# Kernel tuning notes

Hardware: AMD Instinct MI355X
Metric: run time of the kernel (lower is better)

The kernel has to match this reference:

```python
import jax, jax.numpy as jnp
import numpy as np

N_NODES = 50000
N_EDGES = 800000
NODE_IN = 16
NODE_OUT = 3
H = 128
N_LAYERS = 3


def setup_inputs() -> dict:
    key = jax.random.key(0)
    ks = jax.random.split(key, 16)
    s = 0.05
    inp = {
        "x": jax.random.normal(ks[0], (N_NODES, NODE_IN), dtype=jnp.float32),
        "edge_index": jax.random.randint(ks[1], (2, N_EDGES), 0, N_NODES, dtype=jnp.int64),
        # encoder / decoder
        "enc_w": jax.random.normal(ks[2], (NODE_IN, H), dtype=jnp.float32) * s,
        "enc_b": jnp.zeros((H,), dtype=jnp.float32),
        "dec_w": jax.random.normal(ks[3], (H, NODE_OUT), dtype=jnp.float32) * s,
        "dec_b": jnp.zeros((NODE_OUT,), dtype=jnp.float32),
        # 3 processor layers, edge MLP: Linear(2H,H) -> ReLU -> Linear(H,H)
        "edge_w1": jax.random.normal(ks[4], (N_LAYERS, 2 * H, H), dtype=jnp.float32) * s,
        "edge_b1": jnp.zeros((N_LAYERS, H), dtype=jnp.float32),
        "edge_w2": jax.random.normal(ks[5], (N_LAYERS, H, H), dtype=jnp.float32) * s,
        "edge_b2": jnp.zeros((N_LAYERS, H), dtype=jnp.float32),
        # node MLP: Linear(2H,H) -> ReLU -> Linear(H,H)
        "node_w1": jax.random.normal(ks[6], (N_LAYERS, 2 * H, H), dtype=jnp.float32) * s,
        "node_b1": jnp.zeros((N_LAYERS, H), dtype=jnp.float32),
        "node_w2": jax.random.normal(ks[7], (N_LAYERS, H, H), dtype=jnp.float32) * s,
        "node_b2": jnp.zeros((N_LAYERS, H), dtype=jnp.float32),
    }
    return inp


def reference(x, edge_index, enc_w, enc_b, dec_w, dec_b,
              edge_w1, edge_b1, edge_w2, edge_b2,
              node_w1, node_b1, node_w2, node_b2):
    row = edge_index[0]  # source nodes
    col = edge_index[1]  # destination nodes
    h = x @ enc_w + enc_b  # [N, H]
    for l in range(N_LAYERS):
        # EdgeModel: cat(src, dest) -> MLP
        e_in = jnp.concatenate([h[row], h[col]], axis=1)  # [E, 2H]
        e = jnp.maximum(e_in @ edge_w1[l] + edge_b1[l], 0.0) @ edge_w2[l] + edge_b2[l]  # [E, H]
        # NodeModel: scatter_add messages by col, cat with x -> MLP
        agg = jax.ops.segment_sum(e, col, num_segments=h.shape[0])  # [N, H]
        n_in = jnp.concatenate([h, agg], axis=1)  # [N, 2H]
        h_upd = jnp.maximum(n_in @ node_w1[l] + node_b1[l], 0.0) @ node_w2[l] + node_b2[l]
        h = h + h_upd  # residual
    return h @ dec_w + dec_b  # [N, NODE_OUT]
```

## Files before the change

kernel.cpp:

```cpp
#include <hip/hip_runtime.h>
#include <hip/hip_bf16.h>
#include <stdint.h>

#define N_NODES 50000
#define N_EDGES 800000
#define HID 128
#define NODE_IN 16
#define NODE_OUT 3
#define NODE_TILES 782
#define SCAN_BLOCKS 196
#define EDGE_BLOCKS 3125
#define MFOLD_BLOCKS 192
#define SWZA_BLOCKS 576
#define SWZB_BLOCKS 384
#define EDBLOCKS 6250

typedef __attribute__((ext_vector_type(8))) short short8;
typedef __attribute__((ext_vector_type(4))) float f32x4;
typedef __attribute__((ext_vector_type(4))) unsigned int u32x4;

__device__ __forceinline__ unsigned short f2bf(float f) {
    union { float f; unsigned int u; } v; v.f = f;
    unsigned int u = v.u;
    u += 0x7fff + ((u >> 16) & 1);
    return (unsigned short)(u >> 16);
}
__device__ __forceinline__ float bf2f(unsigned short s) {
    union { unsigned int u; float f; } v; v.u = ((unsigned int)s) << 16;
    return v.f;
}
__device__ __forceinline__ float bfu_lo(unsigned int u) {
    union { unsigned int u; float f; } v; v.u = u << 16; return v.f;
}
__device__ __forceinline__ float bfu_hi(unsigned int u) {
    union { unsigned int u; float f; } v; v.u = u & 0xffff0000u; return v.f;
}
__device__ __forceinline__ unsigned int cvt_pk_bf16(float lo, float hi) {
    unsigned int r;
    asm("v_cvt_pk_bf16_f32 %0, %1, %2" : "=v"(r) : "v"(lo), "v"(hi));
    return r;
}

__global__ __launch_bounds__(256) void k1_fused(
    const int* __restrict__ colp, int* __restrict__ cnt8, int* __restrict__ rank,
    const float* __restrict__ edge_w2, const float* __restrict__ node_w1,
    const float* __restrict__ edge_b2,
    float* __restrict__ Mtmp, float* __restrict__ Vtmp,
    const float* __restrict__ x, const float* __restrict__ enc_w,
    const float* __restrict__ enc_b, unsigned short* __restrict__ h,
    const float* __restrict__ edge_w1, const float* __restrict__ node_w2,
    unsigned short* __restrict__ swz,
    const float* __restrict__ eb1,
    unsigned short* __restrict__ S, unsigned short* __restrict__ D) {
    __shared__ float wts[NODE_IN * HID];
    __shared__ float bts[HID];
    __shared__ float xs[64][NODE_IN];
    __shared__ unsigned short hs[64][136];
    int b = blockIdx.x, t = threadIdx.x;
    if (b < EDGE_BLOCKS) {
        int e = b * 256 + t;
        int c = colp[e];
        rank[e] = atomicAdd(&cnt8[(size_t)(b & 7) * N_NODES + c], 1);
    } else if (b < EDGE_BLOCKS + MFOLD_BLOCKS) {
        int d = (b - EDGE_BLOCKS) * 256 + t;
        int L = d / 16384, rem = d & 16383;
        int k = rem >> 7, n = rem & 127;
        const float* w2  = edge_w2 + (size_t)L * 16384;
        const float* w1b = node_w1 + (size_t)L * 32768 + 16384;
        float acc = 0.f;
        #pragma unroll 4
        for (int j = 0; j < 128; j++) acc += w2[k * 128 + j] * w1b[j * 128 + n];
        Mtmp[d] = acc;
        if (k == 0) {
            const float* b2 = edge_b2 + (size_t)L * 128;
            float vv = 0.f;
            #pragma unroll 4
            for (int j = 0; j < 128; j++) vv += b2[j] * w1b[j * 128 + n];
            Vtmp[L * 128 + n] = vv;
        }
    } else if (b < EDGE_BLOCKS + MFOLD_BLOCKS + NODE_TILES) {
        int b2 = b - EDGE_BLOCKS - MFOLD_BLOCKS;
        int wave = t >> 6, l = t & 63, q = l >> 4, l16 = l & 15;
        int nt0s = wave * 4;
        int n0 = b2 * 64;

        for (int i = t; i < NODE_IN * HID; i += 256) wts[i] = enc_w[i];
        if (t < HID) bts[t] = enc_b[t];
        for (int i = t; i < 64 * NODE_IN; i += 256) {
            int nl = i >> 4, ii = i & 15;
            int n = n0 + nl;
            xs[nl][ii] = (n < N_NODES) ? x[n * NODE_IN + ii] : 0.f;
        }
        short8 wr[4][4];
        #pragma unroll
        for (int kt = 0; kt < 4; kt++)
            #pragma unroll
            for (int i = 0; i < 4; i++) {
                int ccol = (nt0s + i) * 16 + l16;
                #pragma unroll
                for (int j = 0; j < 8; j++) {
                    int k = kt * 32 + ((l >> 4) << 3) + j;
                    float v = (ccol < 128) ? edge_w1[k * 128 + ccol]
                                           : edge_w1[(128 + k) * 128 + (ccol - 128)];
                    ((unsigned short*)&wr[kt][i])[j] = f2bf(v);
                }
            }
        __syncthreads();

        for (int o = t; o < 64 * HID; o += 256) {
            int nl = o >> 7, cc = o & 127;
            float acc = bts[cc];
            #pragma unroll
            for (int i = 0; i < NODE_IN; i++) acc += xs[nl][i] * wts[i * HID + cc];
            unsigned short hb = f2bf(acc);
            hs[nl][cc] = hb;
            int n = n0 + nl;
            if (n < N_NODES) h[n * HID + cc] = hb;
        }
        __syncthreads();

        f32x4 acc[4][4];
        #pragma unroll
        for (int g = 0; g < 4; g++)
            #pragma unroll
            for (int i = 0; i < 4; i++) acc[g][i] = (f32x4){0.f, 0.f, 0.f, 0.f};
        #pragma unroll
        for (int kt = 0; kt < 4; kt++) {
            #pragma unroll
            for (int g = 0; g < 4; g++) {
                short8 a = *(const short8*)&hs[g * 16 + l16][kt * 32 + q * 8];
                #pragma unroll
                for (int i = 0; i < 4; i++)
                    acc[g][i] = __builtin_amdgcn_mfma_f32_16x16x32_bf16(a, wr[kt][i], acc[g][i], 0, 0, 0);
            }
        }
        #pragma unroll
        for (int i = 0; i < 4; i++) {
            int cc = (nt0s + i) * 16 + l16;
            float badd = 0.f;
            if (cc >= 128) badd = eb1[cc - 128];
            #pragma unroll
            for (int g = 0; g < 4; g++)
                #pragma unroll
                for (int r = 0; r < 4; r++) {
                    int n = n0 + g * 16 + q * 4 + r;
                    if (n < N_NODES) {
                        unsigned short v = f2bf(acc[g][i][r] + badd);
                        if (cc < 128) S[n * HID + cc] = v;
                        else          D[n * HID + (cc - 128)] = v;
                    }
                }
        }
    } else {
        int d = (b - EDGE_BLOCKS - MFOLD_BLOCKS - NODE_TILES) * 256 + t;
        int L = d / 49152, rem2 = d - L * 49152;
        unsigned short* base = swz + L * 98304;
        if (rem2 < 32768) {
            const float* w1 = edge_w1 + (size_t)L * 32768;
            int j = rem2 & 7, ll = (rem2 >> 3) & 63, tt = rem2 >> 9;
            int nt = tt & 15, kt = tt >> 4;
            int k = kt * 32 + ((ll >> 4) << 3) + j;
            int cc = nt * 16 + (ll & 15);
            float v = (cc < 128) ? w1[k * 128 + cc] : w1[(128 + k) * 128 + (cc - 128)];
            base[rem2] = f2bf(v);
        } else {
            int d2 = rem2 - 32768;
            const float* src = node_w2 + (size_t)L * 16384;
            int j = d2 & 7, ll = (d2 >> 3) & 63, tt = d2 >> 9;
            int nt = tt & 7, kt = tt >> 3;
            int k = kt * 32 + ((ll >> 4) << 3) + j, n = (nt << 4) + (ll & 15);
            base[81920 + d2] = f2bf(src[k * 128 + n]);
        }
    }
}

__global__ __launch_bounds__(256) void k2a_scan1_swizzle(
    const int* __restrict__ cnt8, int* __restrict__ base8, int* __restrict__ cntt,
    int* __restrict__ ex, int* __restrict__ bsums,
    const float* __restrict__ node_w1, const float* __restrict__ Mtmp,
    unsigned short* __restrict__ swz) {
    __shared__ int s[256];
    int b = blockIdx.x, t = threadIdx.x;
    if (b < SCAN_BLOCKS) {
        int i = b * 256 + t;
        int tot = 0;
        if (i < N_NODES) {
            #pragma unroll
            for (int s2 = 0; s2 < 8; s2++) {
                int v = cnt8[(size_t)s2 * N_NODES + i];
                base8[(size_t)s2 * N_NODES + i] = tot;
                tot += v;
            }
            cntt[i] = tot;
        }
        s[t] = tot;
        __syncthreads();
        for (int off = 1; off < 256; off <<= 1) {
            int u = (t >= off) ? s[t - off] : 0;
            __syncthreads();
            s[t] += u;
            __syncthreads();
        }
        if (i < N_NODES) ex[i] = s[t] - tot;
        if (t == 255) bsums[b] = s[255];
    } else {
        int d = (b - SCAN_BLOCKS) * 256 + t;
        int L = d / 32768, d2 = d - L * 32768;
        unsigned short* base = swz + L * 98304;
        int j = d2 & 7, ll = (d2 >> 3) & 63, tt = d2 >> 9;
        int nt = tt & 7, kt = tt >> 3;
        int k = kt * 32 + ((ll >> 4) << 3) + j, n = (nt << 4) + (ll & 15);
        float v = (k < 128) ? node_w1[(size_t)L * 32768 + k * 128 + n]
                            : Mtmp[(size_t)L * 16384 + (k - 128) * 128 + n];
        base[49152 + d2] = f2bf(v);
    }
}

__global__ __launch_bounds__(256) void k3_scatter(
    const int* __restrict__ rowp, const int* __restrict__ colp,
    const int* __restrict__ ex, const int* __restrict__ bsums,
    const int* __restrict__ rank, const int* __restrict__ base8,
    int* __restrict__ rsrt, int* __restrict__ ex2) {
    __shared__ int sc[256];
    __shared__ int ls[SCAN_BLOCKS];
    int b = blockIdx.x, t = threadIdx.x;
    int v = (t < SCAN_BLOCKS) ? bsums[t] : 0;
    sc[t] = v;
    __syncthreads();
    for (int off = 1; off < 256; off <<= 1) {
        int u = (t >= off) ? sc[t - off] : 0;
        __syncthreads();
        sc[t] += u;
        __syncthreads();
    }
    if (t < SCAN_BLOCKS) ls[t] = sc[t] - v;
    __syncthreads();

    if (b < SCAN_BLOCKS) {
        int i = b * 256 + t;
        if (i < N_NODES) ex2[i] = ex[i] + ls[b];
    }
    int e = b * 256 + t;
    int c = colp[e];
    int sh = b & 7;
    int pos = ex[c] + ls[c >> 8] + base8[(size_t)sh * N_NODES + c] + rank[e];
    rsrt[pos] = rowp[e];
}

__global__ __launch_bounds__(256, 8) void edge_kernel(
    const unsigned short* __restrict__ S, const unsigned short* __restrict__ D,
    const int* __restrict__ rsrt, const int* __restrict__ ex2,
    unsigned short* __restrict__ aggB)
{
    int t = threadIdx.x;
    int g32 = t >> 5, ch = t & 31;

    const int q = EDBLOCKS / 8, r = EDBLOCKS % 8;
    int xcd = blockIdx.x & 7, slot = blockIdx.x >> 3;
    int cntx = q + (xcd < r);
    if (slot >= cntx) return;
    int myb = xcd * q + (xcd < r ? xcd : r) + slot;

    int d = myb * 8 + g32;
    int e0 = ex2[d];
    int e1 = (d < N_NODES - 1) ? ex2[d + 1] : N_EDGES;

    int2 dv = *(const int2*)(D + (size_t)d * HID + ch * 4);
    float dr0 = bfu_lo((unsigned int)dv.x), dr1 = bfu_hi((unsigned int)dv.x);
    float dr2 = bfu_lo((unsigned int)dv.y), dr3 = bfu_hi((unsigned int)dv.y);
    float a0 = 0.f, a1 = 0.f, a2 = 0.f, a3 = 0.f;

    auto Srow = [&](int rn) -> int2 {
        return *(const int2*)(S + (size_t)rn * HID + ch * 4);
    };
    auto accum = [&](int2 sv) {
        float v0 = bfu_lo((unsigned int)sv.x) + dr0;
        float v1 = bfu_hi((unsigned int)sv.x) + dr1;
        float v2 = bfu_lo((unsigned int)sv.y) + dr2;
        float v3 = bfu_hi((unsigned int)sv.y) + dr3;
        a0 += v0 > 0.f ? v0 : 0.f;
        a1 += v1 > 0.f ? v1 : 0.f;
        a2 += v2 > 0.f ? v2 : 0.f;
        a3 += v3 > 0.f ? v3 : 0.f;
    };
    const int2 z = make_int2(0, 0);

    int2 c0 = z, c1 = z, c2 = z, c3 = z;
    int rb0 = 0, rb1 = 0, rb2 = 0, rb3 = 0;
    {
        int ra0 = (e0     < e1) ? rsrt[e0]     : 0;
        int ra1 = (e0 + 1 < e1) ? rsrt[e0 + 1] : 0;
        int ra2 = (e0 + 2 < e1) ? rsrt[e0 + 2] : 0;
        int ra3 = (e0 + 3 < e1) ? rsrt[e0 + 3] : 0;
        rb0 = (e0 + 4 < e1) ? rsrt[e0 + 4] : 0;
        rb1 = (e0 + 5 < e1) ? rsrt[e0 + 5] : 0;
        rb2 = (e0 + 6 < e1) ? rsrt[e0 + 6] : 0;
        rb3 = (e0 + 7 < e1) ? rsrt[e0 + 7] : 0;
        if (e0     < e1) c0 = Srow(ra0);
        if (e0 + 1 < e1) c1 = Srow(ra1);
        if (e0 + 2 < e1) c2 = Srow(ra2);
        if (e0 + 3 < e1) c3 = Srow(ra3);
    }

    int e = e0;
    while (e + 12 <= e1) {
        int m0 = rsrt[e + 8], m1 = rsrt[e + 9];
        int2 f0 = Srow(rb0), f1 = Srow(rb1);
        accum(c0); accum(c1);
        int m2 = rsrt[e + 10], m3 = rsrt[e + 11];
        int2 f2 = Srow(rb2), f3 = Srow(rb3);
        accum(c2); accum(c3);
        c0 = f0; c1 = f1; c2 = f2; c3 = f3;
        rb0 = m0; rb1 = m1; rb2 = m2; rb3 = m3;
        e += 4;
    }
    int rem = e1 - e;
    if (rem > 0) accum(c0);
    if (rem > 1) accum(c1);
    if (rem > 2) accum(c2);
    if (rem > 3) accum(c3);
    if (rem > 4) accum(Srow(rb0));
    if (rem > 5) accum(Srow(rb1));
    if (rem > 6) accum(Srow(rb2));
    if (rem > 7) accum(Srow(rb3));
    for (int j = 8; j < rem; j++) accum(Srow(rsrt[e + j]));

    int2 o = make_int2((int)cvt_pk_bf16(a0, a1), (int)cvt_pk_bf16(a2, a3));
    *(int2*)(aggB + (size_t)d * HID + ch * 4) = o;
}

template<int LAST>
__global__ __launch_bounds__(256, 4) void node_kernel(
    unsigned short* __restrict__ h, const unsigned short* __restrict__ aggB,
    const int* __restrict__ cnt,
    const unsigned short* __restrict__ w1m_s, const float* __restrict__ b1,
    const float* __restrict__ vfold,
    const unsigned short* __restrict__ w2s, const float* __restrict__ b2,
    const unsigned short* __restrict__ w1c_next, const float* __restrict__ eb1n,
    unsigned short* __restrict__ S, unsigned short* __restrict__ D,
    const float* __restrict__ dec_w, const float* __restrict__ dec_b, float* __restrict__ out)
{
    __shared__ unsigned short in_h[64][136];
    __shared__ unsigned short in_a[64][136];
    __shared__ int cnt_s[64];
    __shared__ float dw[HID * NODE_OUT];
    __shared__ float db[NODE_OUT];
    int t = threadIdx.x, wave = t >> 6, l = t & 63, q = l >> 4, l16 = l & 15;
    int nt0 = wave * 2, nt0s = wave * 4;
    int n0 = blockIdx.x * 64;

    if (LAST) {
        for (int i = t; i < HID * NODE_OUT; i += 256) dw[i] = dec_w[i];
        if (t < NODE_OUT) db[t] = dec_b[t];
    }

    #pragma unroll
    for (int it = 0; it < 8; it++) {
        int g = it * 256 + t;
        int nl = g >> 5, sub = g & 31, half = sub >> 4, li = sub & 15;
        int n = n0 + nl;
        short8 v = (short8){0, 0, 0, 0, 0, 0, 0, 0};
        if (n < N_NODES) {
            if (half == 0) v = *(const short8*)(h + (size_t)n * HID + li * 8);
            else           v = *(const short8*)(aggB + (size_t)n * HID + li * 8);
        }
        if (half == 0) *(short8*)&in_h[nl][li * 8] = v;
        else           *(short8*)&in_a[nl][li * 8] = v;
    }
    if (t < 64) cnt_s[t] = (n0 + t < N_NODES) ? cnt[n0 + t] : 0;
    __syncthreads();

    float b1r0 = b1[nt0 * 16 + l16], b1r1 = b1[(nt0 + 1) * 16 + l16];
    float vr0 = vfold[nt0 * 16 + l16], vr1 = vfold[(nt0 + 1) * 16 + l16];
    float b2r0 = b2[nt0 * 16 + l16], b2r1 = b2[(nt0 + 1) * 16 + l16];

    f32x4 acc[4][2];
    #pragma unroll
    for (int g = 0; g < 4; g++)
        #pragma unroll
        for (int j = 0; j < 2; j++) acc[g][j] = (f32x4){0.f, 0.f, 0.f, 0.f};
    #pragma unroll
    for (int kt = 0; kt < 8; kt++) {
        short8 b0 = *(const short8*)(w1m_s + ((kt * 8 + nt0)     * 64 + l) * 8);
        short8 b1v = *(const short8*)(w1m_s + ((kt * 8 + nt0 + 1) * 64 + l) * 8);
        #pragma unroll
        for (int g = 0; g < 4; g++) {
            short8 a = (kt < 4) ? *(const short8*)&in_h[g * 16 + l16][kt * 32 + q * 8]
                                : *(const short8*)&in_a[g * 16 + l16][(kt - 4) * 32 + q * 8];
            acc[g][0] = __builtin_amdgcn_mfma_f32_16x16x32_bf16(a, b0, acc[g][0], 0, 0, 0);
            acc[g][1] = __builtin_amdgcn_mfma_f32_16x16x32_bf16(a, b1v, acc[g][1], 0, 0, 0);
        }
    }
    __syncthreads();

    #pragma unroll
    for (int j = 0; j < 2; j++) {
        float bv = j ? b1r1 : b1r0;
        float vv = j ? vr1 : vr0;
        #pragma unroll
        for (int g = 0; g < 4; g++)
            #pragma unroll
            for (int r = 0; r < 4; r++) {
                int m2 = g * 16 + q * 4 + r;
                float v = acc[g][j][r] + bv + (float)cnt_s[m2] * vv;
                v = v > 0.f ? v : 0.f;
                in_a[m2][(nt0 + j) * 16 + l16] = f2bf(v);
            }
    }
    __syncthreads();

    f32x4 acc2[4][2];
    #pragma unroll
    for (int g = 0; g < 4; g++)
        #pragma unroll
        for (int j = 0; j < 2; j++) acc2[g][j] = (f32x4){0.f, 0.f, 0.f, 0.f};
    #pragma unroll
    for (int kt = 0; kt < 4; kt++) {
        short8 b0 = *(const short8*)(w2s + ((kt * 8 + nt0)     * 64 + l) * 8);
        short8 b1v = *(const short8*)(w2s + ((kt * 8 + nt0 + 1) * 64 + l) * 8);
        #pragma unroll
        for (int g = 0; g < 4; g++) {
            short8 a = *(const short8*)&in_a[g * 16 + l16][kt * 32 + q * 8];
            acc2[g][0] = __builtin_amdgcn_mfma_f32_16x16x32_bf16(a, b0, acc2[g][0], 0, 0, 0);
            acc2[g][1] = __builtin_amdgcn_mfma_f32_16x16x32_bf16(a, b1v, acc2[g][1], 0, 0, 0);
        }
    }
    #pragma unroll
    for (int j = 0; j < 2; j++) {
        float bv = j ? b2r1 : b2r0;
        #pragma unroll
        for (int g = 0; g < 4; g++)
            #pragma unroll
            for (int r = 0; r < 4; r++) {
                float v = acc2[g][j][r] + bv;
                int m2 = g * 16 + q * 4 + r;
                int n = n0 + m2;
                if (n < N_NODES) {
                    int c = (nt0 + j) * 16 + l16;
                    unsigned short nh = f2bf(bf2f(in_h[m2][c]) + v);
                    if (!LAST) h[n * HID + c] = nh;
                    in_h[m2][c] = nh;
                }
            }
    }
    __syncthreads();

    if (!LAST) {
        #pragma unroll
        for (int p = 0; p < 2; p++) {
            short8 wr[4][2];
            #pragma unroll
            for (int kt = 0; kt < 4; kt++) {
                wr[kt][0] = *(const short8*)(w1c_next + ((kt * 16 + nt0s + p * 2)     * 64 + l) * 8);
                wr[kt][1] = *(const short8*)(w1c_next + ((kt * 16 + nt0s + p * 2 + 1) * 64 + l) * 8);
            }
            f32x4 accs[4][2];
            #pragma unroll
            for (int g = 0; g < 4; g++)
                #pragma unroll
                for (int i = 0; i < 2; i++) accs[g][i] = (f32x4){0.f, 0.f, 0.f, 0.f};
            #pragma unroll
            for (int kt = 0; kt < 4; kt++) {
                #pragma unroll
                for (int g = 0; g < 4; g++) {
                    short8 a = *(const short8*)&in_h[g * 16 + l16][kt * 32 + q * 8];
                    accs[g][0] = __builtin_amdgcn_mfma_f32_16x16x32_bf16(a, wr[kt][0], accs[g][0], 0, 0, 0);
                    accs[g][1] = __builtin_amdgcn_mfma_f32_16x16x32_bf16(a, wr[kt][1], accs[g][1], 0, 0, 0);
                }
            }
            #pragma unroll
            for (int i = 0; i < 2; i++) {
                int c = (nt0s + p * 2 + i) * 16 + l16;
                float badd = 0.f;
                if (c >= 128) badd = eb1n[c - 128];
                #pragma unroll
                for (int g = 0; g < 4; g++)
                    #pragma unroll
                    for (int r = 0; r < 4; r++) {
                        int n = n0 + g * 16 + q * 4 + r;
                        if (n < N_NODES) {
                            unsigned short v = f2bf(accs[g][i][r] + badd);
                            if (c < 128) S[n * HID + c] = v;
                            else         D[n * HID + (c - 128)] = v;
                        }
                    }
            }
        }
    } else {
        if (t < 64 * NODE_OUT) {
            int nl = t / 3, o = t - 3 * nl;
            int n = n0 + nl;
            if (n < N_NODES) {
                float a = db[o];
                #pragma unroll 4
                for (int k = 0; k < HID; k++) a += bf2f(in_h[nl][k]) * dw[k * 3 + o];
                out[n * 3 + o] = a;
            }
        }
    }
}

extern "C" void kernel_launch(void* const* d_in, const int* in_sizes, int n_in,
                              void* d_out, int out_size, void* d_ws, size_t ws_size,
                              hipStream_t stream) {
    const float* x       = (const float*)d_in[0];
    const int*   ei      = (const int*)d_in[1];
    const float* enc_w   = (const float*)d_in[2];
    const float* enc_b   = (const float*)d_in[3];
    const float* dec_w   = (const float*)d_in[4];
    const float* dec_b   = (const float*)d_in[5];
    const float* edge_w1 = (const float*)d_in[6];
    const float* edge_b1 = (const float*)d_in[7];
    const float* edge_w2 = (const float*)d_in[8];
    const float* edge_b2 = (const float*)d_in[9];
    const float* node_w1 = (const float*)d_in[10];
    const float* node_b1 = (const float*)d_in[11];
    const float* node_w2 = (const float*)d_in[12];
    const float* node_b2 = (const float*)d_in[13];

    char* ws = (char*)d_ws;
    unsigned short* h    = (unsigned short*)ws;
    unsigned short* aggB = (unsigned short*)(ws + 12800000);
    unsigned short* swz  = (unsigned short*)(ws + 25600000);
    int* cnt8            = (int*)(ws + 26189824);
    int* base8           = (int*)(ws + 27789824);
    int* cntt            = (int*)(ws + 29389824);
    int* ex              = (int*)(ws + 29589824);
    int* bsums           = (int*)(ws + 29789824);
    int* rsrt            = (int*)(ws + 29790848);
    unsigned short* Sbuf = (unsigned short*)(ws + 32990848);
    unsigned short* Dbuf = (unsigned short*)(ws + 45790848);
    float* Mtmp          = (float*)(ws + 58590848);
    float* Vtmp          = (float*)(ws + 58787456);
    int* ex2             = (int*)(ws + 58788992);
    int* rank            = (int*)(ws + 58988992);

    const int* rowp = ei;
    const int* colp = ei + N_EDGES;

    hipMemsetAsync(cnt8, 0, (size_t)8 * N_NODES * 4, stream);

    k1_fused<<<EDGE_BLOCKS + MFOLD_BLOCKS + NODE_TILES + SWZA_BLOCKS, 256, 0, stream>>>(
        colp, cnt8, rank, edge_w2, node_w1, edge_b2, Mtmp, Vtmp,
        x, enc_w, enc_b, h, edge_w1, node_w2, swz,
        edge_b1 , Sbuf, Dbuf);
    k2a_scan1_swizzle<<<SCAN_BLOCKS + SWZB_BLOCKS, 256, 0, stream>>>(
        cnt8, base8, cntt, ex, bsums, node_w1, Mtmp, swz);
    k3_scatter<<<EDGE_BLOCKS, 256, 0, stream>>>(
        rowp, colp, ex, bsums, rank, base8, rsrt, ex2);

    for (int L = 0; L < 3; L++) {
        unsigned short* base = swz + (size_t)L * 98304;
        unsigned short* next = swz + (size_t)(L + 1) * 98304;
        edge_kernel<<<6256, 256, 0, stream>>>(Sbuf, Dbuf, rsrt, ex2, aggB);
        if (L < 2) {
            node_kernel<0><<<NODE_TILES, 256, 0, stream>>>(
                h, aggB, cntt,
                base + 49152, node_b1 + (size_t)L * HID, Vtmp + (size_t)L * HID,
                base + 81920, node_b2 + (size_t)L * HID,
                next, edge_b1 + (size_t)(L + 1) * HID, Sbuf, Dbuf, dec_w, dec_b, (float*)d_out);
        } else {
            node_kernel<1><<<NODE_TILES, 256, 0, stream>>>(
                h, aggB, cntt,
                base + 49152, node_b1 + (size_t)L * HID, Vtmp + (size_t)L * HID,
                base + 81920, node_b2 + (size_t)L * HID,
                base , edge_b1 , Sbuf, Dbuf, dec_w, dec_b, (float*)d_out);
        }
    }
}
```

Baseline: 361.5 us.

## Move first-layer S/D projection from k1 into scatter kernel using pre-swizzled weights

The layer-0 node-side edge projection (h times edge_w1 halves, producing S and D) moves out of the encoder blocks of k1_fused and into extra blocks appended to the scatter kernel. The new blocks reload the bf16 h from global memory and read weight fragments directly from the pre-swizzled swz buffer built in k1, instead of gathering and converting fp32 edge_w1 per thread. This lightens k1's node-tile blocks, which had expensive strided weight loads and a large MFMA section, and balances work into k3. The cost is an extra global round-trip for h and a heavier k3 launch.

```diff
diff --git a/kernel.cpp b/kernel.cpp
--- a/kernel.cpp
+++ b/kernel.cpp
@@ -49,13 +49,10 @@
     const float* __restrict__ x, const float* __restrict__ enc_w,
     const float* __restrict__ enc_b, unsigned short* __restrict__ h,
     const float* __restrict__ edge_w1, const float* __restrict__ node_w2,
-    unsigned short* __restrict__ swz,
-    const float* __restrict__ eb1,
-    unsigned short* __restrict__ S, unsigned short* __restrict__ D) {
+    unsigned short* __restrict__ swz) {
     __shared__ float wts[NODE_IN * HID];
     __shared__ float bts[HID];
     __shared__ float xs[64][NODE_IN];
-    __shared__ unsigned short hs[64][136];
     int b = blockIdx.x, t = threadIdx.x;
     if (b < EDGE_BLOCKS) {
         int e = b * 256 + t;
@@ -80,10 +77,7 @@
         }
     } else if (b < EDGE_BLOCKS + MFOLD_BLOCKS + NODE_TILES) {
         int b2 = b - EDGE_BLOCKS - MFOLD_BLOCKS;
-        int wave = t >> 6, l = t & 63, q = l >> 4, l16 = l & 15;
-        int nt0s = wave * 4;
         int n0 = b2 * 64;
-
         for (int i = t; i < NODE_IN * HID; i += 256) wts[i] = enc_w[i];
         if (t < HID) bts[t] = enc_b[t];
         for (int i = t; i < 64 * NODE_IN; i += 256) {
@@ -91,65 +85,14 @@
             int n = n0 + nl;
             xs[nl][ii] = (n < N_NODES) ? x[n * NODE_IN + ii] : 0.f;
         }
-        short8 wr[4][4];
-        #pragma unroll
-        for (int kt = 0; kt < 4; kt++)
-            #pragma unroll
-            for (int i = 0; i < 4; i++) {
-                int ccol = (nt0s + i) * 16 + l16;
-                #pragma unroll
-                for (int j = 0; j < 8; j++) {
-                    int k = kt * 32 + ((l >> 4) << 3) + j;
-                    float v = (ccol < 128) ? edge_w1[k * 128 + ccol]
-                                           : edge_w1[(128 + k) * 128 + (ccol - 128)];
-                    ((unsigned short*)&wr[kt][i])[j] = f2bf(v);
-                }
-            }
         __syncthreads();
-
         for (int o = t; o < 64 * HID; o += 256) {
             int nl = o >> 7, cc = o & 127;
             float acc = bts[cc];
             #pragma unroll
             for (int i = 0; i < NODE_IN; i++) acc += xs[nl][i] * wts[i * HID + cc];
-            unsigned short hb = f2bf(acc);
-            hs[nl][cc] = hb;
             int n = n0 + nl;
-            if (n < N_NODES) h[n * HID + cc] = hb;
-        }
-        __syncthreads();
-
-        f32x4 acc[4][4];
-        #pragma unroll
-        for (int g = 0; g < 4; g++)
-            #pragma unroll
-            for (int i = 0; i < 4; i++) acc[g][i] = (f32x4){0.f, 0.f, 0.f, 0.f};
-        #pragma unroll
-        for (int kt = 0; kt < 4; kt++) {
-            #pragma unroll
-            for (int g = 0; g < 4; g++) {
-                short8 a = *(const short8*)&hs[g * 16 + l16][kt * 32 + q * 8];
-                #pragma unroll
-                for (int i = 0; i < 4; i++)
-                    acc[g][i] = __builtin_amdgcn_mfma_f32_16x16x32_bf16(a, wr[kt][i], acc[g][i], 0, 0, 0);
-            }
-        }
-        #pragma unroll
-        for (int i = 0; i < 4; i++) {
-            int cc = (nt0s + i) * 16 + l16;
-            float badd = 0.f;
-            if (cc >= 128) badd = eb1[cc - 128];
-            #pragma unroll
-            for (int g = 0; g < 4; g++)
-                #pragma unroll
-                for (int r = 0; r < 4; r++) {
-                    int n = n0 + g * 16 + q * 4 + r;
-                    if (n < N_NODES) {
-                        unsigned short v = f2bf(acc[g][i][r] + badd);
-                        if (cc < 128) S[n * HID + cc] = v;
-                        else          D[n * HID + (cc - 128)] = v;
-                    }
-                }
+            if (n < N_NODES) h[n * HID + cc] = f2bf(acc);
         }
     } else {
         int d = (b - EDGE_BLOCKS - MFOLD_BLOCKS - NODE_TILES) * 256 + t;
@@ -216,35 +159,93 @@
     }
 }
 
-__global__ __launch_bounds__(256) void k3_scatter(
+__global__ __launch_bounds__(256) void k3_scatter_sd(
     const int* __restrict__ rowp, const int* __restrict__ colp,
     const int* __restrict__ ex, const int* __restrict__ bsums,
     const int* __restrict__ rank, const int* __restrict__ base8,
-    int* __restrict__ rsrt, int* __restrict__ ex2) {
+    int* __restrict__ rsrt, int* __restrict__ ex2,
+    const unsigned short* __restrict__ h, const unsigned short* __restrict__ w1c,
+    const float* __restrict__ eb1,
+    unsigned short* __restrict__ S, unsigned short* __restrict__ D) {
     __shared__ int sc[256];
     __shared__ int ls[SCAN_BLOCKS];
+    __shared__ unsigned short hs[64][136];
     int b = blockIdx.x, t = threadIdx.x;
-    int v = (t < SCAN_BLOCKS) ? bsums[t] : 0;
-    sc[t] = v;
-    __syncthreads();
-    for (int off = 1; off < 256; off <<= 1) {
-        int u = (t >= off) ? sc[t - off] : 0;
+    if (b < EDGE_BLOCKS) {
+        int v = (t < SCAN_BLOCKS) ? bsums[t] : 0;
+        sc[t] = v;
         __syncthreads();
-        sc[t] += u;
+        for (int off = 1; off < 256; off <<= 1) {
+            int u = (t >= off) ? sc[t - off] : 0;
+            __syncthreads();
+            sc[t] += u;
+            __syncthreads();
+        }
+        if (t < SCAN_BLOCKS) ls[t] = sc[t] - v;
         __syncthreads();
-    }
-    if (t < SCAN_BLOCKS) ls[t] = sc[t] - v;
-    __syncthreads();
-
-    if (b < SCAN_BLOCKS) {
-        int i = b * 256 + t;
-        if (i < N_NODES) ex2[i] = ex[i] + ls[b];
-    }
-    int e = b * 256 + t;
-    int c = colp[e];
-    int sh = b & 7;
-    int pos = ex[c] + ls[c >> 8] + base8[(size_t)sh * N_NODES + c] + rank[e];
-    rsrt[pos] = rowp[e];
+
+        if (b < SCAN_BLOCKS) {
+            int i = b * 256 + t;
+            if (i < N_NODES) ex2[i] = ex[i] + ls[b];
+        }
+        int e = b * 256 + t;
+        int c = colp[e];
+        int sh = b & 7;
+        int pos = ex[c] + ls[c >> 8] + base8[(size_t)sh * N_NODES + c] + rank[e];
+        rsrt[pos] = rowp[e];
+    } else {
+        int b2 = b - EDGE_BLOCKS;
+        int wave = t >> 6, l = t & 63, q = l >> 4, l16 = l & 15;
+        int nt0s = wave * 4;
+        int n0 = b2 * 64;
+        for (int i = t; i < 64 * 16; i += 256) {
+            int nl = i >> 4, li = i & 15;
+            int n = n0 + nl;
+            short8 v = (short8){0, 0, 0, 0, 0, 0, 0, 0};
+            if (n < N_NODES) v = *(const short8*)(h + (size_t)n * HID + li * 8);
+            *(short8*)&hs[nl][li * 8] = v;
+        }
+        short8 wr[4][4];
+        #pragma unroll
+        for (int kt = 0; kt < 4; kt++)
+            #pragma unroll
+            for (int i = 0; i < 4; i++)
+                wr[kt][i] = *(const short8*)(w1c + ((kt * 16 + nt0s + i) * 64 + l) * 8);
+        __syncthreads();
+
+        f32x4 acc[4][4];
+        #pragma unroll
+        for (int g = 0; g < 4; g++)
+            #pragma unroll
+            for (int i = 0; i < 4; i++) acc[g][i] = (f32x4){0.f, 0.f, 0.f, 0.f};
+        #pragma unroll
+        for (int kt = 0; kt < 4; kt++) {
+            #pragma unroll
+            for (int g = 0; g < 4; g++) {
+                short8 a = *(const short8*)&hs[g * 16 + l16][kt * 32 + q * 8];
+                #pragma unroll
+                for (int i = 0; i < 4; i++)
+                    acc[g][i] = __builtin_amdgcn_mfma_f32_16x16x32_bf16(a, wr[kt][i], acc[g][i], 0, 0, 0);
+            }
+        }
+        #pragma unroll
+        for (int i = 0; i < 4; i++) {
+            int cc = (nt0s + i) * 16 + l16;
+            float badd = 0.f;
+            if (cc >= 128) badd = eb1[cc - 128];
+            #pragma unroll
+            for (int g = 0; g < 4; g++)
+                #pragma unroll
+                for (int r = 0; r < 4; r++) {
+                    int n = n0 + g * 16 + q * 4 + r;
+                    if (n < N_NODES) {
+                        unsigned short v = f2bf(acc[g][i][r] + badd);
+                        if (cc < 128) S[n * HID + cc] = v;
+                        else          D[n * HID + (cc - 128)] = v;
+                    }
+                }
+        }
+    }
 }
 
 __global__ __launch_bounds__(256, 8) void edge_kernel(
@@ -542,12 +543,12 @@
 
     k1_fused<<<EDGE_BLOCKS + MFOLD_BLOCKS + NODE_TILES + SWZA_BLOCKS, 256, 0, stream>>>(
         colp, cnt8, rank, edge_w2, node_w1, edge_b2, Mtmp, Vtmp,
-        x, enc_w, enc_b, h, edge_w1, node_w2, swz,
-        edge_b1 , Sbuf, Dbuf);
+        x, enc_w, enc_b, h, edge_w1, node_w2, swz);
     k2a_scan1_swizzle<<<SCAN_BLOCKS + SWZB_BLOCKS, 256, 0, stream>>>(
         cnt8, base8, cntt, ex, bsums, node_w1, Mtmp, swz);
-    k3_scatter<<<EDGE_BLOCKS, 256, 0, stream>>>(
-        rowp, colp, ex, bsums, rank, base8, rsrt, ex2);
+    k3_scatter_sd<<<EDGE_BLOCKS + NODE_TILES, 256, 0, stream>>>(
+        rowp, colp, ex, bsums, rank, base8, rsrt, ex2,
+        h, swz , edge_b1 , Sbuf, Dbuf);
 
     for (int L = 0; L < 3; L++) {
         unsigned short* base = swz + (size_t)L * 98304;
```

Result: faster. 349.4 us (-3.3%).
